# Performance work log

Measured on AMD Instinct MI355X. Metric: run time of the kernel, lower is better.

## Reference

```python
import jax, jax.numpy as jnp
import numpy as np

D_MODEL = 2048
NUM_HEAD = 16
HEAD_DIM = D_MODEL // NUM_HEAD


def setup_inputs() -> dict:
    key = jax.random.key(0)
    ks = jax.random.split(key, 5)
    scale = 1.0 / np.sqrt(D_MODEL)
    x = jax.random.normal(ks[0], (2, 2048, D_MODEL), dtype=jnp.float32)
    wq = jax.random.normal(ks[1], (D_MODEL, D_MODEL), dtype=jnp.float32) * scale
    wk = jax.random.normal(ks[2], (D_MODEL, D_MODEL), dtype=jnp.float32) * scale
    wv = jax.random.normal(ks[3], (D_MODEL, D_MODEL), dtype=jnp.float32) * scale
    wo = jax.random.normal(ks[4], (D_MODEL, D_MODEL), dtype=jnp.float32) * scale
    return {"x": x, "wq": wq, "wk": wk, "wv": wv, "wo": wo}


def _split_heads(t):
    # [B, T, D] -> [B, H, T, dk]
    B, T, _ = t.shape
    return t.reshape(B, T, NUM_HEAD, HEAD_DIM).transpose(0, 2, 1, 3)


def reference(x, wq, wk, wv, wo):
    # nn.Linear computes x @ W.T; weights here are [out, in]
    Q = _split_heads(x @ wq.T)
    K = _split_heads(x @ wk.T)
    V = _split_heads(x @ wv.T)
    scale = 1.0 / jnp.sqrt(jnp.asarray(HEAD_DIM, dtype=x.dtype))
    score = jnp.einsum('bhqd,bhkd->bhqk', Q, K) * scale
    Tq = score.shape[-2]
    causal_mask = jnp.triu(jnp.ones((Tq, Tq), dtype=bool), k=1)
    score = jnp.where(causal_mask, -jnp.inf, score)
    attn = jax.nn.softmax(score, axis=-1)
    out = jnp.einsum('bhqk,bhkd->bhqd', attn, V)
    B, H, T, dk = out.shape
    out = out.transpose(0, 2, 1, 3).reshape(B, T, H * dk)
    return out @ wo.T
```

## Files before the change

kernel.cpp:

```cpp
#include <hip/hip_runtime.h>

#define DM    2048
#define NH    16
#define HD    128
#define TSEQ  2048
#define BATCH 2
#define MROWS (BATCH * TSEQ)

typedef __bf16 bf16_t;
typedef __bf16 bf16x8 __attribute__((ext_vector_type(8)));
typedef __bf16 bf16x4 __attribute__((ext_vector_type(4)));
typedef float  f32x4  __attribute__((ext_vector_type(4)));
typedef float  f32x16 __attribute__((ext_vector_type(16)));
typedef unsigned short u16x8 __attribute__((ext_vector_type(8)));
typedef unsigned int   u32;

static __device__ __forceinline__ unsigned short f2bf_bits(float f) {
  unsigned u = __builtin_bit_cast(unsigned, f);
  u += 0x7fffu + ((u >> 16) & 1u);
  return (unsigned short)(u >> 16);
}
static __device__ __forceinline__ bf16_t f2bf(float f) {
  unsigned short h = f2bf_bits(f);
  return __builtin_bit_cast(bf16_t, h);
}

static __device__ __forceinline__ void gll16(const void* g, void* lds) {
  __builtin_amdgcn_global_load_lds(
      (const __attribute__((address_space(1))) unsigned int*)g,
      (__attribute__((address_space(3))) unsigned int*)lds, 16, 0, 0);
}

static __device__ __forceinline__ float fast_exp2(float x) {
#if __has_builtin(__builtin_amdgcn_exp2f)
  return __builtin_amdgcn_exp2f(x);
#else
  return exp2f(x);
#endif
}
static __device__ __forceinline__ float fast_rcp(float x) {
#if __has_builtin(__builtin_amdgcn_rcpf)
  return __builtin_amdgcn_rcpf(x);
#else
  return 1.0f / x;
#endif
}

static __device__ __forceinline__ u32 cvtpk(float a, float b) {
  u32 d;
  asm("v_cvt_pk_bf16_f32 %0, %1, %2" : "=v"(d) : "v"(a), "v"(b));
  return d;
}
static __device__ __forceinline__ void pl32swap(u32& a, u32& b) {
  asm volatile("v_permlane32_swap_b32 %0, %1" : "+v"(a), "+v"(b));
}

__global__ void cvt_bf16(const float* __restrict__ s, bf16_t* __restrict__ d, int n8) {
  int i = blockIdx.x * blockDim.x + threadIdx.x;
  if (i >= n8) return;
  const float4* sp = reinterpret_cast<const float4*>(s);
  float4 a = sp[2 * i], b = sp[2 * i + 1];
  u16x8 o;
  o[0] = f2bf_bits(a.x); o[1] = f2bf_bits(a.y); o[2] = f2bf_bits(a.z); o[3] = f2bf_bits(a.w);
  o[4] = f2bf_bits(b.x); o[5] = f2bf_bits(b.y); o[6] = f2bf_bits(b.z); o[7] = f2bf_bits(b.w);
  reinterpret_cast<u16x8*>(d)[i] = o;
}

template <int OUTM>
__global__ __launch_bounds__(512, 1) void gemm_3buf(
    const bf16_t* __restrict__ A, const bf16_t* __restrict__ B,
    void* __restrict__ Cq, void* __restrict__ Ck, void* __restrict__ Cv) {
  __shared__ bf16_t Asm[3][256 * 64];
  __shared__ bf16_t Bsm[3][128 * 64];
  const int tid = threadIdx.x;
  const int l = tid & 63, w = tid >> 6;
  const int wm = w >> 1, wn = w & 1;
  const int m0 = blockIdx.y * 256, n0 = blockIdx.x * 128;
  const int NT = DM / 64;

  auto SA = [&](int t, int buf, int s) {
    const int rowbase = s * 64 + w * 8;
    const int row = rowbase + (l >> 3);
    const int ug = (l & 7) ^ (row & 7);
    const int tc = (t < NT) ? t : 0;
    gll16(A + (size_t)(m0 + row) * DM + tc * 64 + ug * 8,
          (char*)Asm[buf] + rowbase * 128);
  };
  auto SB = [&](int t, int buf, int s) {
    const int rowbase = s * 64 + w * 8;
    const int row = rowbase + (l >> 3);
    const int ug = (l & 7) ^ (row & 7);
    const int tc = (t < NT) ? t : 0;
    gll16(B + (size_t)(n0 + row) * DM + tc * 64 + ug * 8,
          (char*)Bsm[buf] + rowbase * 128);
  };

  f32x4 acc[4][4] = {};

#pragma unroll
  for (int s = 0; s < 4; ++s) SA(0, 0, s);
  SB(0, 0, 0); SB(0, 0, 1);
#pragma unroll
  for (int s = 0; s < 4; ++s) SA(1, 1, s);
  SB(1, 1, 0); SB(1, 1, 1);
  asm volatile("s_waitcnt vmcnt(6)" ::: "memory");
  __builtin_amdgcn_s_barrier();
  __builtin_amdgcn_sched_barrier(0);

  for (int j = 0; j < NT; ++j) {
    const int bj = j % 3, bs = (j + 2) % 3;
    const char* Ab_ = (const char*)Asm[bj];
    const char* Bb_ = (const char*)Bsm[bj];
    bf16x8 af[4][2], bfr[4][2];

#pragma unroll
    for (int mi = 0; mi < 4; ++mi)
#pragma unroll
      for (int kh = 0; kh < 2; ++kh) {
        const int row = wm * 64 + mi * 16 + (l & 15);
        const int u = (kh * 4 + (l >> 4)) ^ (row & 7);
        af[mi][kh] = *reinterpret_cast<const bf16x8*>(Ab_ + row * 128 + u * 16);
      }
#pragma unroll
    for (int ni = 0; ni < 4; ++ni)
#pragma unroll
      for (int kh = 0; kh < 2; ++kh) {
        const int row = wn * 64 + ni * 16 + (l & 15);
        const int u = (kh * 4 + (l >> 4)) ^ (row & 7);
        bfr[ni][kh] = *reinterpret_cast<const bf16x8*>(Bb_ + row * 128 + u * 16);
      }

    SA(j + 2, bs, 0); SA(j + 2, bs, 1); SA(j + 2, bs, 2); SA(j + 2, bs, 3);
    SB(j + 2, bs, 0); SB(j + 2, bs, 1);
    __builtin_amdgcn_sched_barrier(0);

    __builtin_amdgcn_s_setprio(1);
#pragma unroll
    for (int kh = 0; kh < 2; ++kh)
#pragma unroll
      for (int mi = 0; mi < 4; ++mi)
#pragma unroll
        for (int ni = 0; ni < 4; ++ni)
          acc[mi][ni] = __builtin_amdgcn_mfma_f32_16x16x32_bf16(
              af[mi][kh], bfr[ni][kh], acc[mi][ni], 0, 0, 0);
    __builtin_amdgcn_s_setprio(0);

    asm volatile("s_waitcnt vmcnt(6)" ::: "memory");
    __builtin_amdgcn_s_barrier();
    __builtin_amdgcn_sched_barrier(0);
  }

  if constexpr (OUTM == 0) {
    const int proj = n0 >> 11;
    const int nc0 = n0 & (DM - 1);
    if (proj < 2) {
      bf16_t* C = (bf16_t*)(proj == 0 ? Cq : Ck);
#pragma unroll
      for (int mi = 0; mi < 4; ++mi) {
        const int row = m0 + wm * 64 + mi * 16 + ((l >> 4) << 2);
#pragma unroll
        for (int ni = 0; ni < 4; ++ni) {
          const int col = nc0 + wn * 64 + ni * 16 + (l & 15);
#pragma unroll
          for (int r = 0; r < 4; ++r)
            C[(size_t)(row + r) * DM + col] = f2bf(acc[mi][ni][r]);
        }
      }
    } else {
      bf16_t* VT = (bf16_t*)Cv;
#pragma unroll
      for (int mi = 0; mi < 4; ++mi) {
        const int row = m0 + wm * 64 + mi * 16 + ((l >> 4) << 2);
        const int bb = row >> 11, tt = row & (TSEQ - 1);
#pragma unroll
        for (int ni = 0; ni < 4; ++ni) {
          const int col = nc0 + wn * 64 + ni * 16 + (l & 15);
          const int hh = col >> 7, dd = col & (HD - 1);
          bf16x4 pk;
#pragma unroll
          for (int r = 0; r < 4; ++r) pk[r] = f2bf(acc[mi][ni][r]);
          *reinterpret_cast<bf16x4*>(VT + (((size_t)bb * NH + hh) * HD + dd) * TSEQ + tt) = pk;
        }
      }
    }
  } else {
    float* C = (float*)Cq;
#pragma unroll
    for (int mi = 0; mi < 4; ++mi) {
      const int row = m0 + wm * 64 + mi * 16 + ((l >> 4) << 2);
#pragma unroll
      for (int ni = 0; ni < 4; ++ni) {
        const int col = n0 + wn * 64 + ni * 16 + (l & 15);
#pragma unroll
        for (int r = 0; r < 4; ++r)
          C[(size_t)(row + r) * DM + col] = acc[mi][ni][r];
      }
    }
  }
}

__global__ __launch_bounds__(256, 2) void flash_attn(
    const bf16_t* __restrict__ Q, const bf16_t* __restrict__ Kx,
    const bf16_t* __restrict__ VT, bf16_t* __restrict__ O) {
  __shared__ bf16_t Ks[2][64 * 128];
  __shared__ bf16_t Vs[2][128 * 64];
  __shared__ float  Ms[4][32];

  const int tid = threadIdx.x;
  const int l = tid & 63, w = tid >> 6;
  const int hi = l >> 5, ln31 = l & 31;
  const int bh = blockIdx.y;
  const int b = bh >> 4, h = bh & 15;
  const size_t base   = ((size_t)b * TSEQ) * DM + (size_t)h * HD;
  const size_t vtbase = ((size_t)b * NH + h) * HD * (size_t)TSEQ;

  auto run_qtile = [&](int qb) {
    const int wq0 = qb * 128 + w * 32;
    const int nt = 2 * qb + 2;

    bf16x8 qf[8];
    {
      const bf16_t* qp = Q + base + (size_t)(wq0 + ln31) * DM + hi * 8;
#pragma unroll
      for (int m = 0; m < 8; ++m)
        qf[m] = *reinterpret_cast<const bf16x8*>(qp + m * 16);
    }

    f32x16 acc[4] = {};
    float mrow = -1e30f, lrow = 0.f;
    const float cc = 0.12752775f;

    auto STAGE = [&](int t, int buf) {
#pragma unroll
      for (int c = 0; c < 4; ++c) {
        const int chunk = w * 4 + c;
        const int krow = chunk * 4 + (l >> 4);
        const int u = l & 15;
        const int ug = (u & 8) | ((u ^ krow) & 7);
        gll16(Kx + base + (size_t)(t * 64 + krow) * DM + ug * 8,
              (char*)Ks[buf] + chunk * 1024);
      }
#pragma unroll
      for (int c = 0; c < 4; ++c) {
        const int ci = w * 4 + c;
        const int d = ci * 8 + (l >> 3);
        const int ug = (l & 7) ^ (l >> 3);
        gll16(VT + vtbase + (size_t)d * TSEQ + t * 64 + ug * 8,
              (char*)Vs[buf] + ci * 1024);
      }
    };

    STAGE(0, 0);
    __syncthreads();
    int cur = 0;

    for (int t = 0; t < nt; ++t) {
      if (t + 1 < nt) STAGE(t + 1, cur ^ 1);

      const bool active = (t * 64 <= wq0 + 31);
      if (active) {
        f32x16 s[2] = {};
        const char* Kb_ = (const char*)Ks[cur];
#pragma unroll
        for (int si = 0; si < 2; ++si) {
          const int kvr = si * 32 + ln31;
#pragma unroll
          for (int m = 0; m < 8; ++m) {
            const int u = 2 * m + hi;
            const int uswz = (u & 8) | ((u ^ kvr) & 7);
            const bf16x8 kf = *reinterpret_cast<const bf16x8*>(Kb_ + kvr * 256 + uswz * 16);
            s[si] = __builtin_amdgcn_mfma_f32_32x32x16_bf16(kf, qf[m], s[si], 0, 0, 0);
          }
        }

        float sv[32];
        const int qg = wq0 + ln31;
#pragma unroll
        for (int si = 0; si < 2; ++si)
#pragma unroll
          for (int r = 0; r < 16; ++r)
            sv[si * 16 + r] = s[si][r] * cc;
        if (t * 64 + 63 > wq0) {
#pragma unroll
          for (int si = 0; si < 2; ++si)
#pragma unroll
            for (int r = 0; r < 16; ++r) {
              const int kvg = t * 64 + si * 32 + (r & 3) + 8 * (r >> 2) + 4 * hi;
              if (kvg > qg) sv[si * 16 + r] = -3.0e38f;
            }
        }

        float mt = sv[0];
#pragma unroll
        for (int r = 1; r < 32; ++r) mt = fmaxf(mt, sv[r]);
        mt = fmaxf(mt, __shfl_xor(mt, 32, 64));

        if (__any(mt > mrow + 8.0f)) {
          const float mn = fmaxf(mrow, mt);
          const float scl = fast_exp2(mrow - mn);
          mrow = mn;
          lrow *= scl;
          if (hi == 0) Ms[w][ln31] = scl;
          float sclg[16];
#pragma unroll
          for (int r = 0; r < 16; ++r)
            sclg[r] = Ms[w][(r & 3) + 8 * (r >> 2) + 4 * hi];
#pragma unroll
          for (int n = 0; n < 4; ++n)
#pragma unroll
            for (int r = 0; r < 16; ++r)
              acc[n][r] *= sclg[r];
        }

        float rs = 0.f;
#pragma unroll
        for (int r = 0; r < 32; ++r) {
          const float p = fast_exp2(sv[r] - mrow);
          sv[r] = p;
          rs += p;
        }
        rs += __shfl_xor(rs, 32, 64);
        lrow += rs;

        u32 frag[4][4];
#pragma unroll
        for (int si = 0; si < 2; ++si) {
#pragma unroll
          for (int half = 0; half < 2; ++half) {
            const float* p = &sv[si * 16 + half * 8];
            u32 a1 = cvtpk(p[0], p[1]);
            u32 b1 = cvtpk(p[4], p[5]);
            pl32swap(a1, b1);
            u32 a2 = cvtpk(p[2], p[3]);
            u32 b2 = cvtpk(p[6], p[7]);
            pl32swap(a2, b2);
            frag[si * 2 + half][0] = a1;
            frag[si * 2 + half][1] = a2;
            frag[si * 2 + half][2] = b1;
            frag[si * 2 + half][3] = b2;
          }
        }

        const char* Vb_ = (const char*)Vs[cur];
#pragma unroll
        for (int ks = 0; ks < 4; ++ks) {
          const bf16x8 pf = __builtin_bit_cast(bf16x8, *reinterpret_cast<u32(*)[4]>(frag[ks]));
#pragma unroll
          for (int n = 0; n < 4; ++n) {
            const int d = n * 32 + ln31;
            const int u = ks * 2 + hi;
            const int uswz = u ^ (d & 7);
            const bf16x8 vf = *reinterpret_cast<const bf16x8*>(Vb_ + d * 128 + uswz * 16);
            acc[n] = __builtin_amdgcn_mfma_f32_32x32x16_bf16(pf, vf, acc[n], 0, 0, 0);
          }
        }
      }
      __syncthreads();
      cur ^= 1;
    }

    if (hi == 0) Ms[w][ln31] = lrow;
    __syncthreads();
    float rl[16];
#pragma unroll
    for (int r = 0; r < 16; ++r)
      rl[r] = fast_rcp(Ms[w][(r & 3) + 8 * (r >> 2) + 4 * hi]);
#pragma unroll
    for (int r = 0; r < 16; ++r) {
      const int q = wq0 + (r & 3) + 8 * (r >> 2) + 4 * hi;
      bf16_t* op = O + base + (size_t)q * DM + ln31;
#pragma unroll
      for (int n = 0; n < 4; ++n)
        op[n * 32] = f2bf(acc[n][r] * rl[r]);
    }
    __syncthreads();
  };

  const int i = blockIdx.x;
  run_qtile(i);
  run_qtile((int)(TSEQ / 128) - 1 - i);
}

extern "C" void kernel_launch(void* const* d_in, const int* in_sizes, int n_in,
                              void* d_out, int out_size, void* d_ws, size_t ws_size,
                              hipStream_t stream) {
  (void)in_sizes; (void)n_in; (void)out_size; (void)ws_size;
  const float* x  = (const float*)d_in[0];
  const float* wq = (const float*)d_in[1];
  const float* wk = (const float*)d_in[2];
  const float* wv = (const float*)d_in[3];
  const float* wo = (const float*)d_in[4];
  float* out = (float*)d_out;

  const size_t nx = (size_t)MROWS * DM;
  const size_t nw = (size_t)DM * DM;
  bf16_t* xb  = (bf16_t*)d_ws;
  bf16_t* wqb = xb + nx;
  bf16_t* wkb = wqb + nw;
  bf16_t* wvb = wkb + nw;
  bf16_t* wob = wvb + nw;
  bf16_t* Qb  = wob + nw;
  bf16_t* Kb  = Qb + nx;
  bf16_t* Vtb = Kb + nx;
  bf16_t* Ab  = Vtb + nx;

  cvt_bf16<<<(int)(nx / 8 / 256), 256, 0, stream>>>(x, xb, (int)(nx / 8));
  cvt_bf16<<<(int)(nw / 8 / 256), 256, 0, stream>>>(wq, wqb, (int)(nw / 8));
  cvt_bf16<<<(int)(nw / 8 / 256), 256, 0, stream>>>(wk, wkb, (int)(nw / 8));
  cvt_bf16<<<(int)(nw / 8 / 256), 256, 0, stream>>>(wv, wvb, (int)(nw / 8));
  cvt_bf16<<<(int)(nw / 8 / 256), 256, 0, stream>>>(wo, wob, (int)(nw / 8));

  gemm_3buf<0><<<dim3(3 * DM / 128, MROWS / 256), 512, 0, stream>>>(
      xb, wqb, Qb, Kb, Vtb);

  flash_attn<<<dim3(TSEQ / 256, BATCH * NH), 256, 0, stream>>>(Qb, Kb, Vtb, Ab);

  gemm_3buf<1><<<dim3(DM / 128, MROWS / 256), 512, 0, stream>>>(
      Ab, wob, out, nullptr, nullptr);
}
```

Before: 246.4 us.

## Split flash attention KV tile across wave pairs and merge partial softmax states

```diff
diff --git a/kernel.cpp b/kernel.cpp
--- a/kernel.cpp
+++ b/kernel.cpp
@@ -64,6 +64,21 @@
   o[0] = f2bf_bits(a.x); o[1] = f2bf_bits(a.y); o[2] = f2bf_bits(a.z); o[3] = f2bf_bits(a.w);
   o[4] = f2bf_bits(b.x); o[5] = f2bf_bits(b.y); o[6] = f2bf_bits(b.z); o[7] = f2bf_bits(b.w);
   reinterpret_cast<u16x8*>(d)[i] = o;
+}
+
+__global__ void cvt_bf16_w4(const float* __restrict__ s0, const float* __restrict__ s1,
+                            const float* __restrict__ s2, const float* __restrict__ s3,
+                            bf16_t* __restrict__ d, int n8seg) {
+  int i = blockIdx.x * blockDim.x + threadIdx.x;
+  if (i >= n8seg) return;
+  const int seg = blockIdx.y;
+  const float* s = (seg == 0) ? s0 : (seg == 1) ? s1 : (seg == 2) ? s2 : s3;
+  const float4* sp = reinterpret_cast<const float4*>(s);
+  float4 a = sp[2 * i], b = sp[2 * i + 1];
+  u16x8 o;
+  o[0] = f2bf_bits(a.x); o[1] = f2bf_bits(a.y); o[2] = f2bf_bits(a.z); o[3] = f2bf_bits(a.w);
+  o[4] = f2bf_bits(b.x); o[5] = f2bf_bits(b.y); o[6] = f2bf_bits(b.z); o[7] = f2bf_bits(b.w);
+  reinterpret_cast<u16x8*>(d + (size_t)seg * DM * DM)[i] = o;
 }
 
 template <int OUTM>
@@ -199,23 +214,24 @@
   }
 }
 
-__global__ __launch_bounds__(256, 2) void flash_attn(
+#define LDS_TOT 75776
+__global__ __launch_bounds__(512, 2) void flash_attn(
     const bf16_t* __restrict__ Q, const bf16_t* __restrict__ Kx,
     const bf16_t* __restrict__ VT, bf16_t* __restrict__ O) {
-  __shared__ bf16_t Ks[2][64 * 128];
-  __shared__ bf16_t Vs[2][128 * 64];
-  __shared__ float  Ms[4][32];
+  __shared__ __align__(16) char Lds[LDS_TOT];
 
   const int tid = threadIdx.x;
   const int l = tid & 63, w = tid >> 6;
   const int hi = l >> 5, ln31 = l & 31;
+  const int qw = w >> 1, kw = w & 1;
   const int bh = blockIdx.y;
   const int b = bh >> 4, h = bh & 15;
   const size_t base   = ((size_t)b * TSEQ) * DM + (size_t)h * HD;
   const size_t vtbase = ((size_t)b * NH + h) * HD * (size_t)TSEQ;
+  const float cc = 0.12752775f;
 
   auto run_qtile = [&](int qb) {
-    const int wq0 = qb * 128 + w * 32;
+    const int wq0 = qb * 128 + qw * 32;
     const int nt = 2 * qb + 2;
 
     bf16x8 qf[8];
@@ -228,25 +244,24 @@
 
     f32x16 acc[4] = {};
     float mrow = -1e30f, lrow = 0.f;
-    const float cc = 0.12752775f;
 
     auto STAGE = [&](int t, int buf) {
 #pragma unroll
-      for (int c = 0; c < 4; ++c) {
-        const int chunk = w * 4 + c;
+      for (int c = 0; c < 2; ++c) {
+        const int chunk = w * 2 + c;
         const int krow = chunk * 4 + (l >> 4);
         const int u = l & 15;
         const int ug = (u & 8) | ((u ^ krow) & 7);
         gll16(Kx + base + (size_t)(t * 64 + krow) * DM + ug * 8,
-              (char*)Ks[buf] + chunk * 1024);
-      }
-#pragma unroll
-      for (int c = 0; c < 4; ++c) {
-        const int ci = w * 4 + c;
+              Lds + buf * 16384 + chunk * 1024);
+      }
+#pragma unroll
+      for (int c = 0; c < 2; ++c) {
+        const int ci = w * 2 + c;
         const int d = ci * 8 + (l >> 3);
         const int ug = (l & 7) ^ (l >> 3);
         gll16(VT + vtbase + (size_t)d * TSEQ + t * 64 + ug * 8,
-              (char*)Vs[buf] + ci * 1024);
+              Lds + 32768 + buf * 16384 + ci * 1024);
       }
     };
 
@@ -257,42 +272,34 @@
     for (int t = 0; t < nt; ++t) {
       if (t + 1 < nt) STAGE(t + 1, cur ^ 1);
 
-      const bool active = (t * 64 <= wq0 + 31);
+      const bool active = (t * 64 + kw * 32 <= wq0 + 31);
       if (active) {
-        f32x16 s[2] = {};
-        const char* Kb_ = (const char*)Ks[cur];
-#pragma unroll
-        for (int si = 0; si < 2; ++si) {
-          const int kvr = si * 32 + ln31;
-#pragma unroll
-          for (int m = 0; m < 8; ++m) {
-            const int u = 2 * m + hi;
-            const int uswz = (u & 8) | ((u ^ kvr) & 7);
-            const bf16x8 kf = *reinterpret_cast<const bf16x8*>(Kb_ + kvr * 256 + uswz * 16);
-            s[si] = __builtin_amdgcn_mfma_f32_32x32x16_bf16(kf, qf[m], s[si], 0, 0, 0);
+        f32x16 s = {};
+        const char* Kb_ = Lds + cur * 16384;
+        const int kvr = kw * 32 + ln31;
+#pragma unroll
+        for (int m = 0; m < 8; ++m) {
+          const int u = 2 * m + hi;
+          const int uswz = (u & 8) | ((u ^ kvr) & 7);
+          const bf16x8 kf = *reinterpret_cast<const bf16x8*>(Kb_ + kvr * 256 + uswz * 16);
+          s = __builtin_amdgcn_mfma_f32_32x32x16_bf16(kf, qf[m], s, 0, 0, 0);
+        }
+
+        float sv[16];
+        const int qg = wq0 + ln31;
+#pragma unroll
+        for (int r = 0; r < 16; ++r) sv[r] = s[r] * cc;
+        if (t * 64 + kw * 32 + 31 > wq0) {
+#pragma unroll
+          for (int r = 0; r < 16; ++r) {
+            const int kvg = t * 64 + kw * 32 + (r & 3) + 8 * (r >> 2) + 4 * hi;
+            if (kvg > qg) sv[r] = -3.0e38f;
           }
         }
 
-        float sv[32];
-        const int qg = wq0 + ln31;
-#pragma unroll
-        for (int si = 0; si < 2; ++si)
-#pragma unroll
-          for (int r = 0; r < 16; ++r)
-            sv[si * 16 + r] = s[si][r] * cc;
-        if (t * 64 + 63 > wq0) {
-#pragma unroll
-          for (int si = 0; si < 2; ++si)
-#pragma unroll
-            for (int r = 0; r < 16; ++r) {
-              const int kvg = t * 64 + si * 32 + (r & 3) + 8 * (r >> 2) + 4 * hi;
-              if (kvg > qg) sv[si * 16 + r] = -3.0e38f;
-            }
-        }
-
         float mt = sv[0];
 #pragma unroll
-        for (int r = 1; r < 32; ++r) mt = fmaxf(mt, sv[r]);
+        for (int r = 1; r < 16; ++r) mt = fmaxf(mt, sv[r]);
         mt = fmaxf(mt, __shfl_xor(mt, 32, 64));
 
         if (__any(mt > mrow + 8.0f)) {
@@ -300,21 +307,16 @@
           const float scl = fast_exp2(mrow - mn);
           mrow = mn;
           lrow *= scl;
-          if (hi == 0) Ms[w][ln31] = scl;
-          float sclg[16];
-#pragma unroll
-          for (int r = 0; r < 16; ++r)
-            sclg[r] = Ms[w][(r & 3) + 8 * (r >> 2) + 4 * hi];
-#pragma unroll
-          for (int n = 0; n < 4; ++n)
-#pragma unroll
-            for (int r = 0; r < 16; ++r)
-              acc[n][r] *= sclg[r];
+#pragma unroll
+          for (int r = 0; r < 16; ++r) {
+            const float sr = __shfl(scl, (r & 3) + 8 * (r >> 2) + 4 * hi, 64);
+            acc[0][r] *= sr; acc[1][r] *= sr; acc[2][r] *= sr; acc[3][r] *= sr;
+          }
         }
 
         float rs = 0.f;
 #pragma unroll
-        for (int r = 0; r < 32; ++r) {
+        for (int r = 0; r < 16; ++r) {
           const float p = fast_exp2(sv[r] - mrow);
           sv[r] = p;
           rs += p;
@@ -322,33 +324,27 @@
         rs += __shfl_xor(rs, 32, 64);
         lrow += rs;
 
-        u32 frag[4][4];
-#pragma unroll
-        for (int si = 0; si < 2; ++si) {
-#pragma unroll
-          for (int half = 0; half < 2; ++half) {
-            const float* p = &sv[si * 16 + half * 8];
-            u32 a1 = cvtpk(p[0], p[1]);
-            u32 b1 = cvtpk(p[4], p[5]);
-            pl32swap(a1, b1);
-            u32 a2 = cvtpk(p[2], p[3]);
-            u32 b2 = cvtpk(p[6], p[7]);
-            pl32swap(a2, b2);
-            frag[si * 2 + half][0] = a1;
-            frag[si * 2 + half][1] = a2;
-            frag[si * 2 + half][2] = b1;
-            frag[si * 2 + half][3] = b2;
-          }
-        }
-
-        const char* Vb_ = (const char*)Vs[cur];
-#pragma unroll
-        for (int ks = 0; ks < 4; ++ks) {
-          const bf16x8 pf = __builtin_bit_cast(bf16x8, *reinterpret_cast<u32(*)[4]>(frag[ks]));
+        u32 frag[2][4];
+#pragma unroll
+        for (int f = 0; f < 2; ++f) {
+          const float* p = &sv[f * 8];
+          u32 a1 = cvtpk(p[0], p[1]);
+          u32 b1 = cvtpk(p[4], p[5]);
+          pl32swap(a1, b1);
+          u32 a2 = cvtpk(p[2], p[3]);
+          u32 b2 = cvtpk(p[6], p[7]);
+          pl32swap(a2, b2);
+          frag[f][0] = a1; frag[f][1] = a2; frag[f][2] = b1; frag[f][3] = b2;
+        }
+
+        const char* Vb_ = Lds + 32768 + cur * 16384;
+#pragma unroll
+        for (int f = 0; f < 2; ++f) {
+          const bf16x8 pf = __builtin_bit_cast(bf16x8, *reinterpret_cast<u32(*)[4]>(frag[f]));
 #pragma unroll
           for (int n = 0; n < 4; ++n) {
             const int d = n * 32 + ln31;
-            const int u = ks * 2 + hi;
+            const int u = (kw * 2 + f) * 2 + hi;
             const int uswz = u ^ (d & 7);
             const bf16x8 vf = *reinterpret_cast<const bf16x8*>(Vb_ + d * 128 + uswz * 16);
             acc[n] = __builtin_amdgcn_mfma_f32_32x32x16_bf16(pf, vf, acc[n], 0, 0, 0);
@@ -359,21 +355,50 @@
       cur ^= 1;
     }
 
-    if (hi == 0) Ms[w][ln31] = lrow;
-    __syncthreads();
-    float rl[16];
-#pragma unroll
-    for (int r = 0; r < 16; ++r)
-      rl[r] = fast_rcp(Ms[w][(r & 3) + 8 * (r >> 2) + 4 * hi]);
-#pragma unroll
-    for (int r = 0; r < 16; ++r) {
-      const int q = wq0 + (r & 3) + 8 * (r >> 2) + 4 * hi;
-      bf16_t* op = O + base + (size_t)q * DM + ln31;
-#pragma unroll
-      for (int n = 0; n < 4; ++n)
-        op[n * 32] = f2bf(acc[n][r] * rl[r]);
+    {
+      float* accb = (float*)(Lds + qw * 16384 + kw * 8192);
+      const int nb = (kw == 0) ? 2 : 0;
+#pragma unroll
+      for (int np = 0; np < 2; ++np) {
+        float* dst = accb + np * 1024;
+#pragma unroll
+        for (int r = 0; r < 16; ++r) {
+          const int row = (r & 3) + 8 * (r >> 2) + 4 * hi;
+          dst[row * 32 + ln31] = acc[nb + np][r];
+        }
+      }
+      float* mlp = (float*)(Lds + 65536 + qw * 1024 + kw * 512);
+      if (hi == 0) { mlp[ln31] = mrow; mlp[32 + ln31] = lrow; }
+      __syncthreads();
+
+      const float* mlo = (float*)(Lds + 65536 + qw * 1024 + (kw ^ 1) * 512);
+      const float mo = mlo[ln31], lo = mlo[32 + ln31];
+      const float mm = fmaxf(mrow, mo);
+      const float as = fast_exp2(mrow - mm);
+      const float ao = fast_exp2(mo - mm);
+      const float rln = fast_rcp(lrow * as + lo * ao);
+      float* ml2p = (float*)(Lds + 69632 + qw * 1536 + kw * 768);
+      if (hi == 0) { ml2p[ln31] = as; ml2p[32 + ln31] = ao; ml2p[64 + ln31] = rln; }
+      __syncthreads();
+
+      const float* accoth = (float*)(Lds + qw * 16384 + (kw ^ 1) * 8192);
+      const int nf = (kw == 0) ? 0 : 2;
+#pragma unroll
+      for (int r = 0; r < 16; ++r) {
+        const int row = (r & 3) + 8 * (r >> 2) + 4 * hi;
+        const float asr = ml2p[row];
+        const float aor = ml2p[32 + row];
+        const float rlr = ml2p[64 + row];
+        const int q = wq0 + row;
+        bf16_t* op = O + base + (size_t)q * DM + ln31;
+#pragma unroll
+        for (int np = 0; np < 2; ++np) {
+          const float vo = (acc[nf + np][r] * asr + accoth[np * 1024 + row * 32 + ln31] * aor) * rlr;
+          op[(kw * 2 + np) * 32] = f2bf(vo);
+        }
+      }
+      __syncthreads();
     }
-    __syncthreads();
   };
 
   const int i = blockIdx.x;
@@ -396,24 +421,20 @@
   const size_t nw = (size_t)DM * DM;
   bf16_t* xb  = (bf16_t*)d_ws;
   bf16_t* wqb = xb + nx;
-  bf16_t* wkb = wqb + nw;
-  bf16_t* wvb = wkb + nw;
-  bf16_t* wob = wvb + nw;
-  bf16_t* Qb  = wob + nw;
+  bf16_t* Qb  = wqb + 4 * nw;
   bf16_t* Kb  = Qb + nx;
   bf16_t* Vtb = Kb + nx;
   bf16_t* Ab  = Vtb + nx;
+  bf16_t* wob = wqb + 3 * nw;
 
   cvt_bf16<<<(int)(nx / 8 / 256), 256, 0, stream>>>(x, xb, (int)(nx / 8));
-  cvt_bf16<<<(int)(nw / 8 / 256), 256, 0, stream>>>(wq, wqb, (int)(nw / 8));
-  cvt_bf16<<<(int)(nw / 8 / 256), 256, 0, stream>>>(wk, wkb, (int)(nw / 8));
-  cvt_bf16<<<(int)(nw / 8 / 256), 256, 0, stream>>>(wv, wvb, (int)(nw / 8));
-  cvt_bf16<<<(int)(nw / 8 / 256), 256, 0, stream>>>(wo, wob, (int)(nw / 8));
+  cvt_bf16_w4<<<dim3((int)(nw / 8 / 256), 4), 256, 0, stream>>>(
+      wq, wk, wv, wo, wqb, (int)(nw / 8));
 
   gemm_3buf<0><<<dim3(3 * DM / 128, MROWS / 256), 512, 0, stream>>>(
       xb, wqb, Qb, Kb, Vtb);
 
-  flash_attn<<<dim3(TSEQ / 256, BATCH * NH), 256, 0, stream>>>(Qb, Kb, Vtb, Ab);
+  flash_attn<<<dim3(TSEQ / 256, BATCH * NH), 512, 0, stream>>>(Qb, Kb, Vtb, Ab);
 
   gemm_3buf<1><<<dim3(DM / 128, MROWS / 256), 512, 0, stream>>>(
       Ab, wob, out, nullptr, nullptr);
```

Measured after the change: 224.1 us. 9.1% less time.
